# Performance work log

Hardware: AMD Instinct MI355X
Metric: run time of the kernel (lower is better)

The kernel has to match this reference:

```python
import jax, jax.numpy as jnp
import numpy as np

B, T, D_IN, H = 1024, 512, 32, 64


def setup_inputs() -> dict:
    key = jax.random.key(0)
    ks = jax.random.split(key, 9)
    s_in = 1.0 / np.sqrt(D_IN)
    s_h = 1.0 / np.sqrt(H)
    return {
        "X": jax.random.normal(ks[0], (B, T, D_IN), dtype=jnp.float32),
        # embed Linear(D_IN -> H), torch layout [out, in]
        "W_emb": jax.random.uniform(ks[1], (H, D_IN), jnp.float32, -s_in, s_in),
        "b_emb": jax.random.uniform(ks[2], (H,), jnp.float32, -s_in, s_in),
        # RNN weights: weight_ih [H,H], weight_hh [H,H], biases [H]
        "W_ih": jax.random.uniform(ks[3], (H, H), jnp.float32, -s_h, s_h),
        "b_ih": jax.random.uniform(ks[4], (H,), jnp.float32, -s_h, s_h),
        "W_hh": jax.random.uniform(ks[5], (H, H), jnp.float32, -s_h, s_h),
        "b_hh": jax.random.uniform(ks[6], (H,), jnp.float32, -s_h, s_h),
        # output Linear(H -> 1)
        "W_out": jax.random.uniform(ks[7], (1, H), jnp.float32, -s_h, s_h),
        "b_out": jax.random.uniform(ks[8], (1,), jnp.float32, -s_h, s_h),
    }


def reference(X, W_emb, b_emb, W_ih, b_ih, W_hh, b_hh, W_out, b_out):
    # embed: [B,T,D_IN] -> [B,T,H]
    emb = jnp.einsum('btd,hd->bth', X, W_emb) + b_emb
    # precompute input-to-hidden contribution for all steps (big GEMM)
    pre = jnp.einsum('bth,gh->btg', emb, W_ih) + b_ih  # [B,T,H]
    h0 = jnp.zeros((X.shape[0], W_hh.shape[0]), dtype=X.dtype)

    def step(h, x_t):
        # torch RNN (tanh): h' = tanh(x W_ih^T + b_ih + h W_hh^T + b_hh)
        h_new = jnp.tanh(x_t + h @ W_hh.T + b_hh)
        return h_new, None

    hT, _ = jax.lax.scan(step, h0, jnp.swapaxes(pre, 0, 1))  # scan over T
    # final FC on last hidden state -> [B]
    return (hT @ W_out.T + b_out)[:, 0]
```

## Files before the change

kernel.cpp:

```cpp
#include <hip/hip_runtime.h>

#define B_DIM 1024
#define T_DIM 512
#define D_IN 32
#define H 64
#define CT 32
#define NCHUNK (T_DIM / CT)

__global__ __attribute__((amdgpu_flat_work_group_size(64, 64),
                          amdgpu_waves_per_eu(1, 1)))
void rnn_kernel(
    const float* __restrict__ X,
    const float* __restrict__ W_emb,
    const float* __restrict__ b_emb,
    const float* __restrict__ W_ih,
    const float* __restrict__ b_ih,
    const float* __restrict__ W_hh,
    const float* __restrict__ b_hh,
    const float* __restrict__ W_out,
    const float* __restrict__ b_out,
    float* __restrict__ out)
{
    __shared__ __align__(16) float wemb[H * D_IN];
    __shared__ __align__(16) float bemb[H];
    __shared__ __align__(16) float xs[2][CT * D_IN];

    const int b = blockIdx.x;
    const int i = threadIdx.x;

    const float* __restrict__ xb = X + (size_t)b * T_DIM * D_IN;

    float4 st0, st1, st2, st3;
    st0 = *(const float4*)&xb[0 * 256 + i * 4];
    st1 = *(const float4*)&xb[1 * 256 + i * 4];
    st2 = *(const float4*)&xb[2 * 256 + i * 4];
    st3 = *(const float4*)&xb[3 * 256 + i * 4];

    #pragma unroll
    for (int k = 0; k < 8; ++k)
        *(float4*)&wemb[k * 256 + i * 4] = *(const float4*)&W_emb[k * 256 + i * 4];
    bemb[i] = b_emb[i];

    float wih[H];
    #pragma unroll
    for (int j = 0; j < H; j += 4) {
        const float4 v = *(const float4*)&W_ih[i * H + j];
        wih[j] = v.x; wih[j + 1] = v.y; wih[j + 2] = v.z; wih[j + 3] = v.w;
    }

    float wc[D_IN];
    #pragma unroll
    for (int d = 0; d < D_IN; ++d) wc[d] = 0.f;
    float ci = b_ih[i] + b_hh[i];
    #pragma unroll 4
    for (int j = 0; j < H; ++j) {
        const float wj = wih[j];
        ci += wj * bemb[j];
        #pragma unroll
        for (int d = 0; d < D_IN; d += 4) {
            const float4 e = *(const float4*)&wemb[j * D_IN + d];
            wc[d]     += wj * e.x;
            wc[d + 1] += wj * e.y;
            wc[d + 2] += wj * e.z;
            wc[d + 3] += wj * e.w;
        }
    }

    float whh[H];
    #pragma unroll
    for (int j = 0; j < H; j += 4) {
        const float4 v = *(const float4*)&W_hh[i * H + j];
        whh[j] = v.x; whh[j + 1] = v.y; whh[j + 2] = v.z; whh[j + 3] = v.w;
    }

    #pragma unroll
    for (int j = 0; j < H; ++j) asm volatile("" : "+v"(whh[j]));
    #pragma unroll
    for (int d = 0; d < D_IN; ++d) asm volatile("" : "+v"(wc[d]));
    asm volatile("" : "+v"(ci));

    *(float4*)&xs[0][0 * 256 + i * 4] = st0;
    *(float4*)&xs[0][1 * 256 + i * 4] = st1;
    *(float4*)&xs[0][2 * 256 + i * 4] = st2;
    *(float4*)&xs[0][3 * 256 + i * 4] = st3;

    float h = 0.f;

    #pragma unroll 1
    for (int c = 0; c < NCHUNK; ++c) {
        const int cur = c & 1;
        float4 pf0, pf1, pf2, pf3;
        if (c + 1 < NCHUNK) {
            const float* __restrict__ nb = &xb[(c + 1) * (CT * D_IN)];
            pf0 = *(const float4*)&nb[0 * 256 + i * 4];
            pf1 = *(const float4*)&nb[1 * 256 + i * 4];
            pf2 = *(const float4*)&nb[2 * 256 + i * 4];
            pf3 = *(const float4*)&nb[3 * 256 + i * 4];
        }

        #pragma unroll 2
        for (int tt = 0; tt < CT; ++tt) {
            const float* __restrict__ xrow = &xs[cur][tt * D_IN];

            const float4 x0 = *(const float4*)&xrow[0];
            const float4 x1 = *(const float4*)&xrow[4];
            const float4 x2 = *(const float4*)&xrow[8];
            const float4 x3 = *(const float4*)&xrow[12];
            const float4 x4 = *(const float4*)&xrow[16];
            const float4 x5 = *(const float4*)&xrow[20];
            const float4 x6 = *(const float4*)&xrow[24];
            const float4 x7 = *(const float4*)&xrow[28];

            float a[8];
            a[0] = ci;
            #pragma unroll
            for (int k = 1; k < 8; ++k) a[k] = 0.f;

            const int hb = __float_as_int(h);
            #pragma unroll
            for (int j = 0; j < H; ++j) {
                const float hj = __int_as_float(__builtin_amdgcn_readlane(hb, j));
                a[j & 7] += whh[j] * hj;
            }

            a[0] += wc[0]  * x0.x;  a[1] += wc[1]  * x0.y;
            a[2] += wc[2]  * x0.z;  a[3] += wc[3]  * x0.w;
            a[4] += wc[4]  * x1.x;  a[5] += wc[5]  * x1.y;
            a[6] += wc[6]  * x1.z;  a[7] += wc[7]  * x1.w;
            a[0] += wc[8]  * x2.x;  a[1] += wc[9]  * x2.y;
            a[2] += wc[10] * x2.z;  a[3] += wc[11] * x2.w;
            a[4] += wc[12] * x3.x;  a[5] += wc[13] * x3.y;
            a[6] += wc[14] * x3.z;  a[7] += wc[15] * x3.w;
            a[0] += wc[16] * x4.x;  a[1] += wc[17] * x4.y;
            a[2] += wc[18] * x4.z;  a[3] += wc[19] * x4.w;
            a[4] += wc[20] * x5.x;  a[5] += wc[21] * x5.y;
            a[6] += wc[22] * x5.z;  a[7] += wc[23] * x5.w;
            a[0] += wc[24] * x6.x;  a[1] += wc[25] * x6.y;
            a[2] += wc[26] * x6.z;  a[3] += wc[27] * x6.w;
            a[4] += wc[28] * x7.x;  a[5] += wc[29] * x7.y;
            a[6] += wc[30] * x7.z;  a[7] += wc[31] * x7.w;

            const float acc = ((a[0] + a[1]) + (a[2] + a[3]))
                            + ((a[4] + a[5]) + (a[6] + a[7]));
            const float e  = __builtin_amdgcn_exp2f(acc * 2.885390081777927f);
            h = __builtin_fmaf(-2.f, __builtin_amdgcn_rcpf(e + 1.f), 1.f);
        }

        if (c + 1 < NCHUNK) {
            const int nxt = cur ^ 1;
            *(float4*)&xs[nxt][0 * 256 + i * 4] = pf0;
            *(float4*)&xs[nxt][1 * 256 + i * 4] = pf1;
            *(float4*)&xs[nxt][2 * 256 + i * 4] = pf2;
            *(float4*)&xs[nxt][3 * 256 + i * 4] = pf3;
        }
    }

    float val = h * W_out[i];
    #pragma unroll
    for (int off = 32; off > 0; off >>= 1)
        val += __shfl_xor(val, off, 64);
    if (i == 0) out[b] = val + b_out[0];
}

extern "C" void kernel_launch(void* const* d_in, const int* in_sizes, int n_in,
                              void* d_out, int out_size, void* d_ws, size_t ws_size,
                              hipStream_t stream) {
    const float* X     = (const float*)d_in[0];
    const float* W_emb = (const float*)d_in[1];
    const float* b_emb = (const float*)d_in[2];
    const float* W_ih  = (const float*)d_in[3];
    const float* b_ih  = (const float*)d_in[4];
    const float* W_hh  = (const float*)d_in[5];
    const float* b_hh  = (const float*)d_in[6];
    const float* W_out = (const float*)d_in[7];
    const float* b_out = (const float*)d_in[8];
    float* out = (float*)d_out;

    rnn_kernel<<<B_DIM, 64, 0, stream>>>(X, W_emb, b_emb, W_ih, b_ih,
                                         W_hh, b_hh, W_out, b_out, out);
}
```

Before: 283.6 us.

## Process two batch rows per wave and broadcast hidden state through LDS

Each 64-thread block now runs two independent batch sequences at once, interleaving their FMA chains to expose more instruction-level parallelism within the serial recurrence. The hidden state is shared through LDS vector reads instead of 64 per-lane readlane broadcasts. In exchange, only half as many waves are launched, so half the SIMDs sit idle. An LDS round trip also now lies on the per-step critical path.

```diff
diff --git a/kernel.cpp b/kernel.cpp
--- a/kernel.cpp
+++ b/kernel.cpp
@@ -6,6 +6,7 @@
 #define H 64
 #define CT 32
 #define NCHUNK (T_DIM / CT)
+#define KB 2
 
 __global__ __attribute__((amdgpu_flat_work_group_size(64, 64),
                           amdgpu_waves_per_eu(1, 1)))
@@ -23,18 +24,25 @@
 {
     __shared__ __align__(16) float wemb[H * D_IN];
     __shared__ __align__(16) float bemb[H];
-    __shared__ __align__(16) float xs[2][CT * D_IN];
-
-    const int b = blockIdx.x;
-    const int i = threadIdx.x;
-
-    const float* __restrict__ xb = X + (size_t)b * T_DIM * D_IN;
-
-    float4 st0, st1, st2, st3;
-    st0 = *(const float4*)&xb[0 * 256 + i * 4];
-    st1 = *(const float4*)&xb[1 * 256 + i * 4];
-    st2 = *(const float4*)&xb[2 * 256 + i * 4];
-    st3 = *(const float4*)&xb[3 * 256 + i * 4];
+    __shared__ __align__(16) float xsA[2][CT * D_IN];
+    __shared__ __align__(16) float xsB[2][CT * D_IN];
+    __shared__ __align__(16) float hsA[H];
+    __shared__ __align__(16) float hsB[H];
+
+    const int i  = threadIdx.x;
+    const int b0 = blockIdx.x * KB;
+
+    const float* __restrict__ xbA = X + (size_t)b0 * T_DIM * D_IN;
+    const float* __restrict__ xbB = X + (size_t)(b0 + 1) * T_DIM * D_IN;
+
+    float4 sA0 = *(const float4*)&xbA[0 * 256 + i * 4];
+    float4 sA1 = *(const float4*)&xbA[1 * 256 + i * 4];
+    float4 sA2 = *(const float4*)&xbA[2 * 256 + i * 4];
+    float4 sA3 = *(const float4*)&xbA[3 * 256 + i * 4];
+    float4 sB0 = *(const float4*)&xbB[0 * 256 + i * 4];
+    float4 sB1 = *(const float4*)&xbB[1 * 256 + i * 4];
+    float4 sB2 = *(const float4*)&xbB[2 * 256 + i * 4];
+    float4 sB3 = *(const float4*)&xbB[3 * 256 + i * 4];
 
     #pragma unroll
     for (int k = 0; k < 8; ++k)
@@ -79,87 +87,112 @@
     for (int d = 0; d < D_IN; ++d) asm volatile("" : "+v"(wc[d]));
     asm volatile("" : "+v"(ci));
 
-    *(float4*)&xs[0][0 * 256 + i * 4] = st0;
-    *(float4*)&xs[0][1 * 256 + i * 4] = st1;
-    *(float4*)&xs[0][2 * 256 + i * 4] = st2;
-    *(float4*)&xs[0][3 * 256 + i * 4] = st3;
-
-    float h = 0.f;
+    *(float4*)&xsA[0][0 * 256 + i * 4] = sA0;
+    *(float4*)&xsA[0][1 * 256 + i * 4] = sA1;
+    *(float4*)&xsA[0][2 * 256 + i * 4] = sA2;
+    *(float4*)&xsA[0][3 * 256 + i * 4] = sA3;
+    *(float4*)&xsB[0][0 * 256 + i * 4] = sB0;
+    *(float4*)&xsB[0][1 * 256 + i * 4] = sB1;
+    *(float4*)&xsB[0][2 * 256 + i * 4] = sB2;
+    *(float4*)&xsB[0][3 * 256 + i * 4] = sB3;
+    hsA[i] = 0.f;
+    hsB[i] = 0.f;
+
+    float hA = 0.f, hB = 0.f;
 
     #pragma unroll 1
     for (int c = 0; c < NCHUNK; ++c) {
         const int cur = c & 1;
-        float4 pf0, pf1, pf2, pf3;
+        float4 pA0, pA1, pA2, pA3, pB0, pB1, pB2, pB3;
         if (c + 1 < NCHUNK) {
-            const float* __restrict__ nb = &xb[(c + 1) * (CT * D_IN)];
-            pf0 = *(const float4*)&nb[0 * 256 + i * 4];
-            pf1 = *(const float4*)&nb[1 * 256 + i * 4];
-            pf2 = *(const float4*)&nb[2 * 256 + i * 4];
-            pf3 = *(const float4*)&nb[3 * 256 + i * 4];
+            const float* __restrict__ nA = &xbA[(c + 1) * (CT * D_IN)];
+            const float* __restrict__ nB = &xbB[(c + 1) * (CT * D_IN)];
+            pA0 = *(const float4*)&nA[0 * 256 + i * 4];
+            pA1 = *(const float4*)&nA[1 * 256 + i * 4];
+            pA2 = *(const float4*)&nA[2 * 256 + i * 4];
+            pA3 = *(const float4*)&nA[3 * 256 + i * 4];
+            pB0 = *(const float4*)&nB[0 * 256 + i * 4];
+            pB1 = *(const float4*)&nB[1 * 256 + i * 4];
+            pB2 = *(const float4*)&nB[2 * 256 + i * 4];
+            pB3 = *(const float4*)&nB[3 * 256 + i * 4];
         }
 
         #pragma unroll 2
         for (int tt = 0; tt < CT; ++tt) {
-            const float* __restrict__ xrow = &xs[cur][tt * D_IN];
-
-            const float4 x0 = *(const float4*)&xrow[0];
-            const float4 x1 = *(const float4*)&xrow[4];
-            const float4 x2 = *(const float4*)&xrow[8];
-            const float4 x3 = *(const float4*)&xrow[12];
-            const float4 x4 = *(const float4*)&xrow[16];
-            const float4 x5 = *(const float4*)&xrow[20];
-            const float4 x6 = *(const float4*)&xrow[24];
-            const float4 x7 = *(const float4*)&xrow[28];
-
-            float a[8];
-            a[0] = ci;
+            const float* __restrict__ xrA = &xsA[cur][tt * D_IN];
+            const float* __restrict__ xrB = &xsB[cur][tt * D_IN];
+
+            float aA0 = ci, aA1 = 0.f, aA2 = 0.f, aA3 = 0.f;
+            float aB0 = ci, aB1 = 0.f, aB2 = 0.f, aB3 = 0.f;
+
             #pragma unroll
-            for (int k = 1; k < 8; ++k) a[k] = 0.f;
-
-            const int hb = __float_as_int(h);
+            for (int d = 0; d < D_IN; d += 8) {
+                const float4 xa0 = *(const float4*)&xrA[d];
+                const float4 xa1 = *(const float4*)&xrA[d + 4];
+                const float4 xb0 = *(const float4*)&xrB[d];
+                const float4 xb1 = *(const float4*)&xrB[d + 4];
+                aA0 += wc[d]     * xa0.x;  aA1 += wc[d + 1] * xa0.y;
+                aA2 += wc[d + 2] * xa0.z;  aA3 += wc[d + 3] * xa0.w;
+                aB0 += wc[d]     * xb0.x;  aB1 += wc[d + 1] * xb0.y;
+                aB2 += wc[d + 2] * xb0.z;  aB3 += wc[d + 3] * xb0.w;
+                aA0 += wc[d + 4] * xa1.x;  aA1 += wc[d + 5] * xa1.y;
+                aA2 += wc[d + 6] * xa1.z;  aA3 += wc[d + 7] * xa1.w;
+                aB0 += wc[d + 4] * xb1.x;  aB1 += wc[d + 5] * xb1.y;
+                aB2 += wc[d + 6] * xb1.z;  aB3 += wc[d + 7] * xb1.w;
+            }
+
             #pragma unroll
-            for (int j = 0; j < H; ++j) {
-                const float hj = __int_as_float(__builtin_amdgcn_readlane(hb, j));
-                a[j & 7] += whh[j] * hj;
+            for (int j = 0; j < H; j += 8) {
+                const float4 ha0 = *(const float4*)&hsA[j];
+                const float4 ha1 = *(const float4*)&hsA[j + 4];
+                const float4 hb0 = *(const float4*)&hsB[j];
+                const float4 hb1 = *(const float4*)&hsB[j + 4];
+                aA0 += whh[j]     * ha0.x;  aA1 += whh[j + 1] * ha0.y;
+                aA2 += whh[j + 2] * ha0.z;  aA3 += whh[j + 3] * ha0.w;
+                aB0 += whh[j]     * hb0.x;  aB1 += whh[j + 1] * hb0.y;
+                aB2 += whh[j + 2] * hb0.z;  aB3 += whh[j + 3] * hb0.w;
+                aA0 += whh[j + 4] * ha1.x;  aA1 += whh[j + 5] * ha1.y;
+                aA2 += whh[j + 6] * ha1.z;  aA3 += whh[j + 7] * ha1.w;
+                aB0 += whh[j + 4] * hb1.x;  aB1 += whh[j + 5] * hb1.y;
+                aB2 += whh[j + 6] * hb1.z;  aB3 += whh[j + 7] * hb1.w;
             }
 
-            a[0] += wc[0]  * x0.x;  a[1] += wc[1]  * x0.y;
-            a[2] += wc[2]  * x0.z;  a[3] += wc[3]  * x0.w;
-            a[4] += wc[4]  * x1.x;  a[5] += wc[5]  * x1.y;
-            a[6] += wc[6]  * x1.z;  a[7] += wc[7]  * x1.w;
-            a[0] += wc[8]  * x2.x;  a[1] += wc[9]  * x2.y;
-            a[2] += wc[10] * x2.z;  a[3] += wc[11] * x2.w;
-            a[4] += wc[12] * x3.x;  a[5] += wc[13] * x3.y;
-            a[6] += wc[14] * x3.z;  a[7] += wc[15] * x3.w;
-            a[0] += wc[16] * x4.x;  a[1] += wc[17] * x4.y;
-            a[2] += wc[18] * x4.z;  a[3] += wc[19] * x4.w;
-            a[4] += wc[20] * x5.x;  a[5] += wc[21] * x5.y;
-            a[6] += wc[22] * x5.z;  a[7] += wc[23] * x5.w;
-            a[0] += wc[24] * x6.x;  a[1] += wc[25] * x6.y;
-            a[2] += wc[26] * x6.z;  a[3] += wc[27] * x6.w;
-            a[4] += wc[28] * x7.x;  a[5] += wc[29] * x7.y;
-            a[6] += wc[30] * x7.z;  a[7] += wc[31] * x7.w;
-
-            const float acc = ((a[0] + a[1]) + (a[2] + a[3]))
-                            + ((a[4] + a[5]) + (a[6] + a[7]));
-            const float e  = __builtin_amdgcn_exp2f(acc * 2.885390081777927f);
-            h = __builtin_fmaf(-2.f, __builtin_amdgcn_rcpf(e + 1.f), 1.f);
+            const float accA = (aA0 + aA1) + (aA2 + aA3);
+            const float accB = (aB0 + aB1) + (aB2 + aB3);
+            const float eA = __builtin_amdgcn_exp2f(accA * 2.885390081777927f);
+            const float eB = __builtin_amdgcn_exp2f(accB * 2.885390081777927f);
+            hA = __builtin_fmaf(-2.f, __builtin_amdgcn_rcpf(eA + 1.f), 1.f);
+            hB = __builtin_fmaf(-2.f, __builtin_amdgcn_rcpf(eB + 1.f), 1.f);
+            hsA[i] = hA;
+            hsB[i] = hB;
         }
 
         if (c + 1 < NCHUNK) {
             const int nxt = cur ^ 1;
-            *(float4*)&xs[nxt][0 * 256 + i * 4] = pf0;
-            *(float4*)&xs[nxt][1 * 256 + i * 4] = pf1;
-            *(float4*)&xs[nxt][2 * 256 + i * 4] = pf2;
-            *(float4*)&xs[nxt][3 * 256 + i * 4] = pf3;
-        }
-    }
-
-    float val = h * W_out[i];
-    #pragma unroll
-    for (int off = 32; off > 0; off >>= 1)
-        val += __shfl_xor(val, off, 64);
-    if (i == 0) out[b] = val + b_out[0];
+            *(float4*)&xsA[nxt][0 * 256 + i * 4] = pA0;
+            *(float4*)&xsA[nxt][1 * 256 + i * 4] = pA1;
+            *(float4*)&xsA[nxt][2 * 256 + i * 4] = pA2;
+            *(float4*)&xsA[nxt][3 * 256 + i * 4] = pA3;
+            *(float4*)&xsB[nxt][0 * 256 + i * 4] = pB0;
+            *(float4*)&xsB[nxt][1 * 256 + i * 4] = pB1;
+            *(float4*)&xsB[nxt][2 * 256 + i * 4] = pB2;
+            *(float4*)&xsB[nxt][3 * 256 + i * 4] = pB3;
+        }
+    }
+
+    const float wo = W_out[i];
+    float vA = hA * wo;
+    float vB = hB * wo;
+    #pragma unroll
+    for (int off = 32; off > 0; off >>= 1) {
+        vA += __shfl_xor(vA, off, 64);
+        vB += __shfl_xor(vB, off, 64);
+    }
+    if (i == 0) {
+        const float bo = b_out[0];
+        out[b0]     = vA + bo;
+        out[b0 + 1] = vB + bo;
+    }
 }
 
 extern "C" void kernel_launch(void* const* d_in, const int* in_sizes, int n_in,
@@ -176,6 +209,6 @@
     const float* b_out = (const float*)d_in[8];
     float* out = (float*)d_out;
 
-    rnn_kernel<<<B_DIM, 64, 0, stream>>>(X, W_emb, b_emb, W_ih, b_ih,
-                                         W_hh, b_hh, W_out, b_out, out);
+    rnn_kernel<<<B_DIM / KB, 64, 0, stream>>>(X, W_emb, b_emb, W_ih, b_ih,
+                                              W_hh, b_hh, W_out, b_out, out);
 }
```

New measurement: 579.5 us. +104.3%, slower.
